# Optimization experiments

Measured on AMD Instinct MI355X. Metric: run time of the kernel, lower is better.

The kernel has to match this reference:

```python
import jax, jax.numpy as jnp
import numpy as np
import math

E = 256          # embed_dims
H = 8            # num_heads
ITER = 2         # iterative steps
PC_RANGE = (-140.8, -40.0, -3.0, 140.8, 40.0, 1.0)


def sine_embed(pos, num_feats):
    # pos: (..., 3) in (0,1); returns (..., 3*num_feats), per-coord interleaved sin/cos
    scale = 2.0 * math.pi
    i = jnp.arange(num_feats, dtype=jnp.float32)
    dim_t = 10000.0 ** (2.0 * jnp.floor(i / 2.0) / num_feats)
    p = pos[..., None] * scale / dim_t                      # (..., 3, F)
    emb = jnp.stack([jnp.sin(p[..., 0::2]), jnp.cos(p[..., 1::2])], axis=-1)
    emb = emb.reshape(p.shape[:-1] + (num_feats,))          # (..., 3, F)
    return emb.reshape(pos.shape[:-1] + (3 * num_feats,))


def mha(q, k, v, Wi, bi, Wo, bo, n_heads):
    # torch nn.MultiheadAttention math, seq-first layout: q (L,N,C), k/v (M,N,C)
    L, N, C = q.shape
    D = C // n_heads
    qp = (q @ Wi[:C].T + bi[:C]).reshape(L, N, n_heads, D)
    kp = (k @ Wi[C:2 * C].T + bi[C:2 * C]).reshape(k.shape[0], N, n_heads, D)
    vp = (v @ Wi[2 * C:].T + bi[2 * C:]).reshape(v.shape[0], N, n_heads, D)
    scores = jnp.einsum('lnhd,mnhd->nhlm', qp, kp) / math.sqrt(D)
    attn = jax.nn.softmax(scores, axis=-1)
    o = jnp.einsum('nhlm,mnhd->lnhd', attn, vp).reshape(L, N, C)
    return o @ Wo.T + bo


def setup_inputs() -> dict:
    key = jax.random.key(0)
    ks = jax.random.split(key, 12)
    Q, TOT, B, LMAX = 2048, 40, 8, 5
    s = 0.02
    return {
        'x': jax.random.normal(ks[0], (Q, TOT, E), jnp.float32),
        'reference_points': jax.random.uniform(ks[1], (TOT, Q, 3), jnp.float32),
        'pairwise_t_matrix': jax.random.normal(ks[2], (B, LMAX, LMAX, 4, 4), jnp.float32),
        'record_len': np.full((B,), 5, dtype=np.int64),
        'in_proj_w': jax.random.normal(ks[3], (3 * E, E), jnp.float32) * s,
        'in_proj_b': jnp.zeros((3 * E,), jnp.float32),
        'out_w': jax.random.normal(ks[4], (E, E), jnp.float32) * s,
        'out_b': jnp.zeros((E,), jnp.float32),
        'bev_w1': jax.random.normal(ks[5], (E, 3 * E), jnp.float32) * s,
        'bev_b1': jnp.zeros((E,), jnp.float32),
        'bev_w2': jax.random.normal(ks[6], (E, E), jnp.float32) * s,
        'bev_b2': jnp.zeros((E,), jnp.float32),
    }


def reference(x, reference_points, pairwise_t_matrix, in_proj_w, in_proj_b,
              out_w, out_b, bev_w1, bev_b1, bev_w2, bev_b2, record_len):
    rl = np.asarray(record_len)
    offsets = np.concatenate([[0], np.cumsum(rl)]).astype(int)
    lo = jnp.asarray(PC_RANGE[:3], jnp.float32)
    hi = jnp.asarray(PC_RANGE[3:], jnp.float32)

    x_cav = jnp.transpose(x, (1, 0, 2))                    # (total_cav, Q, C)
    ref = reference_points * (hi - lo) + lo                # un-normalize to pc_range

    outs = []
    for b in range(len(rl)):
        s, e = offsets[b], offsets[b + 1]
        n = e - s
        b_x = x_cav[s:e]                                   # (n, Q, C)
        if n == 1:
            outs.append(b_x)
            continue
        b_ref = ref[s:e]                                   # (n, Q, 3)
        t_ego = pairwise_t_matrix[b, :n, 0]                # (n, 4, 4) transform-to-ego
        homo = jnp.concatenate([b_ref, jnp.ones(b_ref.shape[:-1] + (1,), b_ref.dtype)], axis=-1)
        trans = jax.nn.sigmoid(jnp.einsum('nij,nqj->nqi', t_ego, homo)[..., :3])
        pe = sine_embed(trans, E)                          # (n, Q, 3E)
        bev = jax.nn.relu(pe @ bev_w1.T + bev_b1) @ bev_w2.T + bev_b2  # (n, Q, C)

        ego = b_x[0:1]
        neigh = b_x[1:]                                    # (n-1, Q, C)
        kk = neigh + bev[1:]
        for _ in range(ITER):
            q = jnp.broadcast_to(ego, neigh.shape)
            o = q + mha(q, kk, neigh, in_proj_w, in_proj_b, out_w, out_b, H)
            ego = jnp.sum(o, axis=0, keepdims=True)
        outs.append(jnp.concatenate([ego, neigh], axis=0))

    out = jnp.concatenate(outs, axis=0)                    # (total_cav, Q, C)
    return jnp.transpose(out, (1, 0, 2))                   # (Q, total_cav, C)
```

## Files before the change

kernel.cpp:

```cpp
#include <hip/hip_runtime.h>
#include <cstdint>
#include <cstddef>

typedef __bf16 bf16;
typedef __attribute__((ext_vector_type(8))) __bf16 bf16x8;
typedef __attribute__((ext_vector_type(4))) float f32x4;
typedef __attribute__((ext_vector_type(4))) unsigned int u32x4;

#define QN 2048

#if __has_builtin(__builtin_amdgcn_sinf)
#define SIN_REV(x) __builtin_amdgcn_sinf(x)
#define COS_REV(x) __builtin_amdgcn_cosf(x)
#else
#define SIN_REV(x) __sinf((x) * 6.283185307179586f)
#define COS_REV(x) __cosf((x) * 6.283185307179586f)
#endif

__device__ __forceinline__ float sigmoidf_(float v) { return 1.0f / (1.0f + __expf(-v)); }

__device__ __forceinline__ bf16x8 cvt8(const float* p) {
  const f32x4* p4 = (const f32x4*)p;
  f32x4 lo = p4[0], hi = p4[1];
  bf16x8 r;
#pragma unroll
  for (int j = 0; j < 4; ++j) { r[j] = (bf16)lo[j]; r[j + 4] = (bf16)hi[j]; }
  return r;
}

__device__ __forceinline__ void load_lds16(const bf16* g, bf16* l) {
  __builtin_amdgcn_global_load_lds(
      (const __attribute__((address_space(1))) void*)g,
      (__attribute__((address_space(3))) void*)l, 16, 0, 0);
}

__global__ __launch_bounds__(256) void setup_ker(
    const float* __restrict__ ipw, const float* __restrict__ ow,
    const float* __restrict__ w1, bf16* __restrict__ wb,
    const float* __restrict__ ipb, const float* __restrict__ w2f,
    const float* __restrict__ b2f, bf16* __restrict__ Wc,
    float* __restrict__ bkf) {
  __shared__ float row[256];
  __shared__ float red[256];
  if (blockIdx.x < 224) {
    int e = (blockIdx.x * 256 + threadIdx.x) * 8;
    const float* src; int off;
    if (e < 196608)      { src = ipw; off = e; }
    else if (e < 262144) { src = ow;  off = e - 196608; }
    else                 { src = w1;  off = e - 262144; }
    *(bf16x8*)(wb + e) = cvt8(src + off);
    return;
  }
  const int j = blockIdx.x - 224, l = threadIdx.x;
  row[l] = ipw[65536 + j * 256 + l];
  __syncthreads();
  float acc = 0.f;
#pragma unroll 4
  for (int m = 0; m < 256; ++m) acc += row[m] * w2f[m * 256 + l];
  Wc[(size_t)j * 512 + l] = (bf16)acc;
  Wc[(size_t)j * 512 + 256 + l] = (bf16)row[l];
  red[l] = row[l] * b2f[l];
  __syncthreads();
  for (int s = 128; s > 0; s >>= 1) {
    if (l < s) red[l] += red[l + s];
    __syncthreads();
  }
  if (l == 0) bkf[j] = ipb[256 + j] + red[0];
}

__global__ __launch_bounds__(256) void mega_ker(
    const bf16* __restrict__ w1b, const float* __restrict__ b1,
    const bf16* __restrict__ Wc, const float* __restrict__ bkf,
    const bf16* __restrict__ wv, const float* __restrict__ bv,
    const float* __restrict__ x, const float* __restrict__ rp,
    const float* __restrict__ pm, bf16* __restrict__ kp,
    bf16* __restrict__ vp, float* __restrict__ out) {
  __shared__ bf16 As[64][40];
  __shared__ bf16 Bs[256][32];
  __shared__ bf16 hT[64][256];

  const int tid = threadIdx.x;
  const int wave = tid >> 6, lane = tid & 63;
  const int m16 = lane & 15, quad = lane >> 4;
  const int sRow = tid >> 2, sq = tid & 3;

  if (blockIdx.x >= 2048) {
    for (int i = (blockIdx.x - 2048) * 256 + tid; i < 5242880; i += 524288) {
      int t = (i >> 6) % 40;
      if ((t % 5) != 0) ((u32x4*)out)[i] = ((const u32x4*)x)[i];
    }
    return;
  }

  const bool isPE = blockIdx.x < 1024;
  const int rowBase = (isPE ? blockIdx.x : blockIdx.x - 1024) << 6;
  const int rgA = rowBase + sRow;
  const int b = rgA >> 13, j = (rgA >> 11) & 3, q = rgA & 2047;
  const float* afp = x + (((size_t)q * 40 + b * 5 + 1 + j) << 8);

  f32x4 acc[4][4] = {};

  if (isPE) {
    const int t = b * 5 + 1 + j;
    const float* rpp = rp + ((size_t)t * QN + q) * 3;
    float r0 = rpp[0] * 281.6f - 140.8f;
    float r1 = rpp[1] * 80.0f - 40.0f;
    float r2 = rpp[2] * 4.0f - 3.0f;
    const float* T = pm + (size_t)t * 80;
    const float tr0 = sigmoidf_(T[0] * r0 + T[1] * r1 + T[2] * r2 + T[3]);
    const float tr1 = sigmoidf_(T[4] * r0 + T[5] * r1 + T[6] * r2 + T[7]);
    const float tr2 = sigmoidf_(T[8] * r0 + T[9] * r1 + T[10] * r2 + T[11]);

    const bf16* ws1 = w1b + (size_t)((wave << 6) + (lane >> 2)) * 768 + ((lane & 3) << 3);
    for (int k0 = 0; k0 < 768; k0 += 32) {
#pragma unroll
      for (int i = 0; i < 4; ++i)
        load_lds16(ws1 + (size_t)(i << 4) * 768 + k0, &Bs[(wave << 6) + (i << 4)][0]);
      bf16x8 a0;
      {
        int c = k0 >> 8;
        float tc = (c == 0) ? tr0 : (c == 1 ? tr1 : tr2);
        int ti0 = ((k0 & 255) + (sq << 3)) >> 1;
        float freq = exp2f((float)ti0 * -0.10381025296522975f);
#pragma unroll
        for (int p = 0; p < 4; ++p) {
          float ang = tc * freq;
          a0[2 * p]     = (bf16)SIN_REV(ang);
          a0[2 * p + 1] = (bf16)COS_REV(ang);
          freq *= 0.93057204092467f;
        }
      }
      *(bf16x8*)(&As[sRow][sq << 3]) = a0;
      __syncthreads();
      bf16x8 afr[4], bfr[4];
#pragma unroll
      for (int mt = 0; mt < 4; ++mt)
        afr[mt] = *(const bf16x8*)(&As[(mt << 4) + m16][quad << 3]);
#pragma unroll
      for (int nt = 0; nt < 4; ++nt)
        bfr[nt] = *(const bf16x8*)(&Bs[(wave << 6) + (nt << 4) + m16][quad << 3]);
#pragma unroll
      for (int mt = 0; mt < 4; ++mt)
#pragma unroll
        for (int nt = 0; nt < 4; ++nt)
          acc[mt][nt] = __builtin_amdgcn_mfma_f32_16x16x32_bf16(
              afr[mt], bfr[nt], acc[mt][nt], 0, 0, 0);
      __syncthreads();
    }
#pragma unroll
    for (int mt = 0; mt < 4; ++mt)
#pragma unroll
      for (int nt = 0; nt < 4; ++nt) {
        const int col = (wave << 6) + (nt << 4) + m16;
        const float bvv = b1[col];
#pragma unroll
        for (int rg = 0; rg < 4; ++rg) {
          const int row = (mt << 4) + (quad << 2) + rg;
          hT[row][((((col >> 3) ^ (row & 7)) << 3) + (col & 7))] =
              (bf16)fmaxf(acc[mt][nt][rg] + bvv, 0.0f);
        }
      }
    __syncthreads();

#pragma unroll
    for (int mt = 0; mt < 4; ++mt)
#pragma unroll
      for (int nt = 0; nt < 4; ++nt) {
        f32x4 z = {0.f, 0.f, 0.f, 0.f};
        acc[mt][nt] = z;
      }
    const bf16* ws2 = Wc + (size_t)((wave << 6) + (lane >> 2)) * 512 + ((lane & 3) << 3);
    for (int k0 = 0; k0 < 512; k0 += 32) {
#pragma unroll
      for (int i = 0; i < 4; ++i)
        load_lds16(ws2 + (size_t)(i << 4) * 512 + k0, &Bs[(wave << 6) + (i << 4)][0]);
      if (k0 >= 256) {
        bf16x8 a0 = cvt8(afp + (k0 - 256) + (sq << 3));
        *(bf16x8*)(&As[sRow][sq << 3]) = a0;
      }
      __syncthreads();
      bf16x8 afr[4], bfr[4];
      if (k0 < 256) {
#pragma unroll
        for (int mt = 0; mt < 4; ++mt) {
          const int row = (mt << 4) + m16;
          afr[mt] = *(const bf16x8*)(
              &hT[row][((((k0 >> 3) + quad) ^ (row & 7)) << 3)]);
        }
      } else {
#pragma unroll
        for (int mt = 0; mt < 4; ++mt)
          afr[mt] = *(const bf16x8*)(&As[(mt << 4) + m16][quad << 3]);
      }
#pragma unroll
      for (int nt = 0; nt < 4; ++nt)
        bfr[nt] = *(const bf16x8*)(&Bs[(wave << 6) + (nt << 4) + m16][quad << 3]);
#pragma unroll
      for (int mt = 0; mt < 4; ++mt)
#pragma unroll
        for (int nt = 0; nt < 4; ++nt)
          acc[mt][nt] = __builtin_amdgcn_mfma_f32_16x16x32_bf16(
              afr[mt], bfr[nt], acc[mt][nt], 0, 0, 0);
      __syncthreads();
    }
#pragma unroll
    for (int mt = 0; mt < 4; ++mt)
#pragma unroll
      for (int nt = 0; nt < 4; ++nt) {
        const int col = (wave << 6) + (nt << 4) + m16;
        const float bvv = bkf[col];
#pragma unroll
        for (int rg = 0; rg < 4; ++rg) {
          const int r = rowBase + (mt << 4) + (quad << 2) + rg;
          kp[(size_t)r * 256 + col] = (bf16)(acc[mt][nt][rg] + bvv);
        }
      }
    return;
  }

  const bf16* wsV = wv + (size_t)((wave << 6) + (lane >> 2)) * 256 + ((lane & 3) << 3);
  for (int k0 = 0; k0 < 256; k0 += 32) {
#pragma unroll
    for (int i = 0; i < 4; ++i)
      load_lds16(wsV + (size_t)(i << 4) * 256 + k0, &Bs[(wave << 6) + (i << 4)][0]);
    bf16x8 a0 = cvt8(afp + k0 + (sq << 3));
    *(bf16x8*)(&As[sRow][sq << 3]) = a0;
    __syncthreads();
    bf16x8 afr[4], bfr[4];
#pragma unroll
    for (int mt = 0; mt < 4; ++mt)
      afr[mt] = *(const bf16x8*)(&As[(mt << 4) + m16][quad << 3]);
#pragma unroll
    for (int nt = 0; nt < 4; ++nt)
      bfr[nt] = *(const bf16x8*)(&Bs[(wave << 6) + (nt << 4) + m16][quad << 3]);
#pragma unroll
    for (int mt = 0; mt < 4; ++mt)
#pragma unroll
      for (int nt = 0; nt < 4; ++nt)
        acc[mt][nt] = __builtin_amdgcn_mfma_f32_16x16x32_bf16(
            afr[mt], bfr[nt], acc[mt][nt], 0, 0, 0);
    __syncthreads();
  }
#pragma unroll
  for (int mt = 0; mt < 4; ++mt)
#pragma unroll
    for (int nt = 0; nt < 4; ++nt) {
      const int col = (wave << 6) + (nt << 4) + m16;
      const float bvv = bv[col];
#pragma unroll
      for (int rg = 0; rg < 4; ++rg) {
        const int r = rowBase + (mt << 4) + (quad << 2) + rg;
        vp[(size_t)r * 256 + col] = (bf16)(acc[mt][nt][rg] + bvv);
      }
    }
}

__device__ __forceinline__ void proj32db(const bf16 (*AP)[256],
                                         bf16 (*BsP)[256][32],
                                         const bf16* __restrict__ WB,
                                         f32x4 (*acc)[4], int wave, int lane) {
  const int m16 = lane & 15, quad = lane >> 4;
#define PSTAGE(P_, K_)                                                        \
  { _Pragma("unroll") for (int i_ = 0; i_ < 4; ++i_) {                        \
      const bf16* src_ = WB +                                                 \
          (size_t)((wave << 6) + (i_ << 4) + (lane >> 2)) * 256 + (K_) +      \
          ((lane & 3) << 3);                                                  \
      load_lds16(src_, &BsP[P_][(wave << 6) + (i_ << 4)][0]); } }
  PSTAGE(0, 0);
#pragma unroll
  for (int t = 0; t < 8; ++t) {
    const int p = t & 1;
    if (t < 7) {
      PSTAGE(p ^ 1, (t + 1) << 5);
      asm volatile("s_waitcnt vmcnt(4)" ::: "memory");
    } else {
      asm volatile("s_waitcnt vmcnt(0)" ::: "memory");
    }
    __builtin_amdgcn_sched_barrier(0);
    const int k0 = t << 5;
    bf16x8 afr[2], bfr[4];
#pragma unroll
    for (int mt = 0; mt < 2; ++mt) {
      const int r = (mt << 4) + m16;
      afr[mt] = *(const bf16x8*)(&AP[r][(((k0 >> 3) + quad) ^ (r & 7)) << 3]);
    }
#pragma unroll
    for (int nt = 0; nt < 4; ++nt)
      bfr[nt] = *(const bf16x8*)(&BsP[p][(wave << 6) + (nt << 4) + m16][quad << 3]);
#pragma unroll
    for (int mt = 0; mt < 2; ++mt)
#pragma unroll
      for (int nt = 0; nt < 4; ++nt)
        acc[mt][nt] = __builtin_amdgcn_mfma_f32_16x16x32_bf16(
            afr[mt], bfr[nt], acc[mt][nt], 0, 0, 0);
  }
#undef PSTAGE
}

__device__ __forceinline__ void attn_phase(bf16 (*P)[256],
                                           const bf16* __restrict__ kp,
                                           const bf16* __restrict__ vp,
                                           int rowBase, int tid) {
  const int r = tid >> 3, h = tid & 7;
  const int re = rowBase + r, b = re >> 11, q = re & 2047;
  float qv[32];
#pragma unroll
  for (int i = 0; i < 4; ++i) {
    bf16x8 t = *(const bf16x8*)(&P[r][((((h << 2) + i)) ^ (r & 7)) << 3]);
#pragma unroll
    for (int j = 0; j < 8; ++j) qv[i * 8 + j] = (float)t[j];
  }
  const size_t base = ((size_t)(b * 4) * QN + q) * 256 + h * 32;
  float s[4];
#pragma unroll
  for (int m = 0; m < 4; ++m) {
    const bf16x8* kv = (const bf16x8*)(kp + base + (size_t)m * (QN * 256));
    float a = 0.f;
#pragma unroll
    for (int i = 0; i < 4; ++i) {
      bf16x8 t = kv[i];
#pragma unroll
      for (int j = 0; j < 8; ++j) a += qv[i * 8 + j] * (float)t[j];
    }
    s[m] = a * 0.17677669529663687f;
  }
  float mx = fmaxf(fmaxf(s[0], s[1]), fmaxf(s[2], s[3]));
  float e0 = __expf(s[0] - mx), e1 = __expf(s[1] - mx);
  float e2 = __expf(s[2] - mx), e3 = __expf(s[3] - mx);
  float inv = 1.0f / (e0 + e1 + e2 + e3);
  float w[4] = {e0 * inv, e1 * inv, e2 * inv, e3 * inv};
  float ov[32] = {};
#pragma unroll
  for (int m = 0; m < 4; ++m) {
    const bf16x8* vv = (const bf16x8*)(vp + base + (size_t)m * (QN * 256));
#pragma unroll
    for (int i = 0; i < 4; ++i) {
      bf16x8 t = vv[i];
#pragma unroll
      for (int j = 0; j < 8; ++j) ov[i * 8 + j] += w[m] * (float)t[j];
    }
  }
#pragma unroll
  for (int i = 0; i < 4; ++i) {
    bf16x8 t;
#pragma unroll
    for (int j = 0; j < 8; ++j) t[j] = (bf16)ov[i * 8 + j];
    *(bf16x8*)(&P[r][((((h << 2) + i)) ^ (r & 7)) << 3]) = t;
  }
}

__global__ __launch_bounds__(256, 2) void iter_ker(
    const bf16* __restrict__ kp, const bf16* __restrict__ vp,
    const bf16* __restrict__ wq, const bf16* __restrict__ owb,
    const float* __restrict__ qb, const float* __restrict__ ob,
    const float* __restrict__ x, float* __restrict__ out) {
  __shared__ bf16 P1[32][256];
  __shared__ bf16 P2[32][256];
  __shared__ bf16 Bs[2][256][32];

  const int tid = threadIdx.x;
  const int rowBase = blockIdx.x << 5;
  const int wave = tid >> 6, lane = tid & 63;
  const int m16 = lane & 15, quad = lane >> 4;

  {
    const int r = tid >> 3, e = tid & 7;
    const int re = rowBase + r, b = re >> 11, q = re & 2047;
    const float* src = x + (((size_t)q * 40 + b * 5) << 8) + (e << 5);
#pragma unroll
    for (int s = 0; s < 4; ++s) {
      bf16x8 v = cvt8(src + s * 8);
      *(bf16x8*)(&P1[r][((((e << 2) + s)) ^ (r & 7)) << 3]) = v;
    }
  }
  __syncthreads();

  float e1r[2][4][4];
  f32x4 acc[2][4];

#define ZACC                                                                  \
  { _Pragma("unroll") for (int mt = 0; mt < 2; ++mt)                          \
    _Pragma("unroll") for (int nt = 0; nt < 4; ++nt) {                        \
      f32x4 z = {0.f, 0.f, 0.f, 0.f}; acc[mt][nt] = z; } }

#define QEPI                                                                  \
  { _Pragma("unroll") for (int mt = 0; mt < 2; ++mt)                          \
    _Pragma("unroll") for (int nt = 0; nt < 4; ++nt) {                        \
      const int col = (wave << 6) + (nt << 4) + m16;                          \
      const float bv = qb[col];                                               \
      _Pragma("unroll") for (int rg = 0; rg < 4; ++rg) {                      \
        const int row = (mt << 4) + (quad << 2) + rg;                         \
        P2[row][(((col >> 3) ^ (row & 7)) << 3) + (col & 7)] =                \
            (bf16)(acc[mt][nt][rg] + bv);                                     \
      } } }

  ZACC;
  proj32db(P1, Bs, wq, acc, wave, lane);
  QEPI;
  __syncthreads();
  attn_phase(P2, kp, vp, rowBase, tid);
  __syncthreads();
  ZACC;
  proj32db(P2, Bs, owb, acc, wave, lane);
#pragma unroll
  for (int mt = 0; mt < 2; ++mt)
#pragma unroll
    for (int nt = 0; nt < 4; ++nt) {
      const int col = (wave << 6) + (nt << 4) + m16;
      const float bv = ob[col];
#pragma unroll
      for (int rg = 0; rg < 4; ++rg) {
        const int row = (mt << 4) + (quad << 2) + rg;
        const int re = rowBase + row, b = re >> 11, q = re & 2047;
        float xe = x[(((size_t)q * 40 + b * 5) << 8) + col];
        float e1 = 4.0f * (xe + acc[mt][nt][rg] + bv);
        e1r[mt][nt][rg] = e1;
        P1[row][(((col >> 3) ^ (row & 7)) << 3) + (col & 7)] = (bf16)e1;
      }
    }
  __syncthreads();

  ZACC;
  proj32db(P1, Bs, wq, acc, wave, lane);
  QEPI;
  __syncthreads();
  attn_phase(P2, kp, vp, rowBase, tid);
  __syncthreads();
  ZACC;
  proj32db(P2, Bs, owb, acc, wave, lane);
#pragma unroll
  for (int mt = 0; mt < 2; ++mt)
#pragma unroll
    for (int nt = 0; nt < 4; ++nt) {
      const int col = (wave << 6) + (nt << 4) + m16;
      const float bv = ob[col];
#pragma unroll
      for (int rg = 0; rg < 4; ++rg) {
        const int row = (mt << 4) + (quad << 2) + rg;
        const int re = rowBase + row, b = re >> 11, q = re & 2047;
        out[(((size_t)q * 40 + b * 5) << 8) + col] =
            4.0f * (e1r[mt][nt][rg] + acc[mt][nt][rg] + bv);
      }
    }
#undef ZACC
#undef QEPI
}

extern "C" void kernel_launch(void* const* d_in, const int* in_sizes, int n_in,
                              void* d_out, int out_size, void* d_ws, size_t ws_size,
                              hipStream_t stream) {
  (void)n_in; (void)out_size; (void)ws_size;
  const float* x   = (const float*)d_in[0];
  const float* rp  = (const float*)d_in[1];
  const float* pm  = (const float*)d_in[2];
  const int wbase = (in_sizes[3] == 8) ? 4 : 3;
  const float* ipw = (const float*)d_in[wbase + 0];
  const float* ipb = (const float*)d_in[wbase + 1];
  const float* ow  = (const float*)d_in[wbase + 2];
  const float* obv = (const float*)d_in[wbase + 3];
  const float* w1  = (const float*)d_in[wbase + 4];
  const float* b1  = (const float*)d_in[wbase + 5];
  const float* w2  = (const float*)d_in[wbase + 6];
  const float* b2  = (const float*)d_in[wbase + 7];
  float* out = (float*)d_out;
  char* ws = (char*)d_ws;

  bf16* kp   = (bf16*)(ws + 33554432);
  bf16* vp   = (bf16*)(ws + 67108864);
  bf16* wb   = (bf16*)(ws + 100663296);
  bf16* Wc   = (bf16*)(ws + 101711872);
  float* bkf = (float*)(ws + 101974016);
  const bf16* wq  = wb;
  const bf16* wv  = wb + 131072;
  const bf16* owb = wb + 196608;
  const bf16* w1b = wb + 262144;

  setup_ker<<<480, 256, 0, stream>>>(ipw, ow, w1, wb, ipb, w2, b2, Wc, bkf);
  mega_ker<<<4096, 256, 0, stream>>>(w1b, b1, Wc, bkf, wv, ipb + 512,
                                     x, rp, pm, kp, vp, out);
  iter_ker<<<512, 256, 0, stream>>>(kp, vp, wq, owb, ipb, obv, x, out);
}
```

Measured before the change: 341.0 us.

## Double-buffer weight tiles and compute sine features in registers to drop barriers

The PE GEMM phases now double-buffer the per-wave B tiles in shared memory and prefetch the next k-slice while computing the current one. Because each wave reads only the B rows it loaded itself, the block barriers are replaced by vmcnt waits. The sine/cosine positional features are computed straight into MFMA A-fragments per lane rather than staged through shared memory. This removes per-iteration __syncthreads and the LDS round trip, at the cost of redundant transcendental work per lane (4 rows each), extra LDS for the second buffer, and reliance on hand-written waitcnt ordering.

```diff
diff --git a/kernel.cpp b/kernel.cpp
--- a/kernel.cpp
+++ b/kernel.cpp
@@ -76,7 +76,7 @@
     const float* __restrict__ pm, bf16* __restrict__ kp,
     bf16* __restrict__ vp, float* __restrict__ out) {
   __shared__ bf16 As[64][40];
-  __shared__ bf16 Bs[256][32];
+  __shared__ bf16 BsD[2][256][32];
   __shared__ bf16 hT[64][256];
 
   const int tid = threadIdx.x;
@@ -94,59 +94,70 @@
 
   const bool isPE = blockIdx.x < 1024;
   const int rowBase = (isPE ? blockIdx.x : blockIdx.x - 1024) << 6;
-  const int rgA = rowBase + sRow;
-  const int b = rgA >> 13, j = (rgA >> 11) & 3, q = rgA & 2047;
-  const float* afp = x + (((size_t)q * 40 + b * 5 + 1 + j) << 8);
 
   f32x4 acc[4][4] = {};
 
   if (isPE) {
-    const int t = b * 5 + 1 + j;
-    const float* rpp = rp + ((size_t)t * QN + q) * 3;
-    float r0 = rpp[0] * 281.6f - 140.8f;
-    float r1 = rpp[1] * 80.0f - 40.0f;
-    float r2 = rpp[2] * 4.0f - 3.0f;
-    const float* T = pm + (size_t)t * 80;
-    const float tr0 = sigmoidf_(T[0] * r0 + T[1] * r1 + T[2] * r2 + T[3]);
-    const float tr1 = sigmoidf_(T[4] * r0 + T[5] * r1 + T[6] * r2 + T[7]);
-    const float tr2 = sigmoidf_(T[8] * r0 + T[9] * r1 + T[10] * r2 + T[11]);
+    float trL[3][4];
+#pragma unroll
+    for (int mt = 0; mt < 4; ++mt) {
+      const int rr = rowBase + (mt << 4) + m16;
+      const int bb = rr >> 13, jj = (rr >> 11) & 3, qq = rr & 2047;
+      const int tt = bb * 5 + 1 + jj;
+      const float* rpp = rp + ((size_t)tt * QN + qq) * 3;
+      float r0 = rpp[0] * 281.6f - 140.8f;
+      float r1 = rpp[1] * 80.0f - 40.0f;
+      float r2 = rpp[2] * 4.0f - 3.0f;
+      const float* T = pm + (size_t)tt * 80;
+      trL[0][mt] = sigmoidf_(T[0] * r0 + T[1] * r1 + T[2] * r2 + T[3]);
+      trL[1][mt] = sigmoidf_(T[4] * r0 + T[5] * r1 + T[6] * r2 + T[7]);
+      trL[2][mt] = sigmoidf_(T[8] * r0 + T[9] * r1 + T[10] * r2 + T[11]);
+    }
 
     const bf16* ws1 = w1b + (size_t)((wave << 6) + (lane >> 2)) * 768 + ((lane & 3) << 3);
-    for (int k0 = 0; k0 < 768; k0 += 32) {
-#pragma unroll
-      for (int i = 0; i < 4; ++i)
-        load_lds16(ws1 + (size_t)(i << 4) * 768 + k0, &Bs[(wave << 6) + (i << 4)][0]);
-      bf16x8 a0;
-      {
-        int c = k0 >> 8;
-        float tc = (c == 0) ? tr0 : (c == 1 ? tr1 : tr2);
-        int ti0 = ((k0 & 255) + (sq << 3)) >> 1;
-        float freq = exp2f((float)ti0 * -0.10381025296522975f);
-#pragma unroll
-        for (int p = 0; p < 4; ++p) {
+#define STG1(P_, K_)                                                          \
+    { _Pragma("unroll") for (int i_ = 0; i_ < 4; ++i_)                        \
+        load_lds16(ws1 + (size_t)(i_ << 4) * 768 + (K_),                      \
+                   &BsD[P_][(wave << 6) + (i_ << 4)][0]); }
+    STG1(0, 0);
+#pragma unroll
+    for (int t = 0; t < 24; ++t) {
+      const int p = t & 1;
+      if (t < 23) {
+        STG1(p ^ 1, (t + 1) << 5);
+        asm volatile("s_waitcnt vmcnt(4)" ::: "memory");
+      } else {
+        asm volatile("s_waitcnt vmcnt(0)" ::: "memory");
+      }
+      __builtin_amdgcn_sched_barrier(0);
+      const int k0 = t << 5;
+      const int c = k0 >> 8;
+      bf16x8 afr[4], bfr[4];
+#pragma unroll
+      for (int mt = 0; mt < 4; ++mt) {
+        const float tc = trL[c][mt];
+        float freq = exp2f((float)((((k0 & 255)) + (quad << 3)) >> 1) *
+                           -0.10381025296522975f);
+#pragma unroll
+        for (int pp = 0; pp < 4; ++pp) {
           float ang = tc * freq;
-          a0[2 * p]     = (bf16)SIN_REV(ang);
-          a0[2 * p + 1] = (bf16)COS_REV(ang);
+          afr[mt][2 * pp]     = (bf16)SIN_REV(ang);
+          afr[mt][2 * pp + 1] = (bf16)COS_REV(ang);
           freq *= 0.93057204092467f;
         }
       }
-      *(bf16x8*)(&As[sRow][sq << 3]) = a0;
-      __syncthreads();
-      bf16x8 afr[4], bfr[4];
-#pragma unroll
-      for (int mt = 0; mt < 4; ++mt)
-        afr[mt] = *(const bf16x8*)(&As[(mt << 4) + m16][quad << 3]);
 #pragma unroll
       for (int nt = 0; nt < 4; ++nt)
-        bfr[nt] = *(const bf16x8*)(&Bs[(wave << 6) + (nt << 4) + m16][quad << 3]);
+        bfr[nt] = *(const bf16x8*)(&BsD[p][(wave << 6) + (nt << 4) + m16][quad << 3]);
 #pragma unroll
       for (int mt = 0; mt < 4; ++mt)
 #pragma unroll
         for (int nt = 0; nt < 4; ++nt)
           acc[mt][nt] = __builtin_amdgcn_mfma_f32_16x16x32_bf16(
               afr[mt], bfr[nt], acc[mt][nt], 0, 0, 0);
-      __syncthreads();
-    }
+    }
+#undef STG1
+
 #pragma unroll
     for (int mt = 0; mt < 4; ++mt)
 #pragma unroll
@@ -170,38 +181,68 @@
         acc[mt][nt] = z;
       }
     const bf16* ws2 = Wc + (size_t)((wave << 6) + (lane >> 2)) * 512 + ((lane & 3) << 3);
-    for (int k0 = 0; k0 < 512; k0 += 32) {
-#pragma unroll
-      for (int i = 0; i < 4; ++i)
-        load_lds16(ws2 + (size_t)(i << 4) * 512 + k0, &Bs[(wave << 6) + (i << 4)][0]);
-      if (k0 >= 256) {
-        bf16x8 a0 = cvt8(afp + (k0 - 256) + (sq << 3));
-        *(bf16x8*)(&As[sRow][sq << 3]) = a0;
-      }
-      __syncthreads();
+#define STG2(P_, K_)                                                          \
+    { _Pragma("unroll") for (int i_ = 0; i_ < 4; ++i_)                        \
+        load_lds16(ws2 + (size_t)(i_ << 4) * 512 + (K_),                      \
+                   &BsD[P_][(wave << 6) + (i_ << 4)][0]); }
+    STG2(0, 0);
+#pragma unroll
+    for (int t = 0; t < 8; ++t) {
+      const int p = t & 1;
+      if (t < 7) {
+        STG2(p ^ 1, (t + 1) << 5);
+        asm volatile("s_waitcnt vmcnt(4)" ::: "memory");
+      } else {
+        asm volatile("s_waitcnt vmcnt(0)" ::: "memory");
+      }
+      __builtin_amdgcn_sched_barrier(0);
+      const int k0 = t << 5;
       bf16x8 afr[4], bfr[4];
-      if (k0 < 256) {
-#pragma unroll
-        for (int mt = 0; mt < 4; ++mt) {
-          const int row = (mt << 4) + m16;
-          afr[mt] = *(const bf16x8*)(
-              &hT[row][((((k0 >> 3) + quad) ^ (row & 7)) << 3)]);
-        }
-      } else {
-#pragma unroll
-        for (int mt = 0; mt < 4; ++mt)
-          afr[mt] = *(const bf16x8*)(&As[(mt << 4) + m16][quad << 3]);
+#pragma unroll
+      for (int mt = 0; mt < 4; ++mt) {
+        const int row = (mt << 4) + m16;
+        afr[mt] = *(const bf16x8*)(
+            &hT[row][((((k0 >> 3) + quad) ^ (row & 7)) << 3)]);
       }
 #pragma unroll
       for (int nt = 0; nt < 4; ++nt)
-        bfr[nt] = *(const bf16x8*)(&Bs[(wave << 6) + (nt << 4) + m16][quad << 3]);
+        bfr[nt] = *(const bf16x8*)(&BsD[p][(wave << 6) + (nt << 4) + m16][quad << 3]);
 #pragma unroll
       for (int mt = 0; mt < 4; ++mt)
 #pragma unroll
         for (int nt = 0; nt < 4; ++nt)
           acc[mt][nt] = __builtin_amdgcn_mfma_f32_16x16x32_bf16(
               afr[mt], bfr[nt], acc[mt][nt], 0, 0, 0);
-      __syncthreads();
+    }
+#undef STG2
+
+    {
+      const int rgA = rowBase + sRow;
+      const int b = rgA >> 13, j = (rgA >> 11) & 3, q = rgA & 2047;
+      const float* afp = x + (((size_t)q * 40 + b * 5 + 1 + j) << 8);
+      for (int k0 = 256; k0 < 512; k0 += 32) {
+#pragma unroll
+        for (int i = 0; i < 4; ++i)
+          load_lds16(ws2 + (size_t)(i << 4) * 512 + k0,
+                     &BsD[0][(wave << 6) + (i << 4)][0]);
+        bf16x8 a0 = cvt8(afp + (k0 - 256) + (sq << 3));
+        *(bf16x8*)(&As[sRow][sq << 3]) = a0;
+        __syncthreads();
+        bf16x8 afr[4], bfr[4];
+#pragma unroll
+        for (int mt = 0; mt < 4; ++mt)
+          afr[mt] = *(const bf16x8*)(&As[(mt << 4) + m16][quad << 3]);
+#pragma unroll
+        for (int nt = 0; nt < 4; ++nt)
+          bfr[nt] = *(const bf16x8*)(&BsD[0][(wave << 6) + (nt << 4) + m16][quad << 3]);
+#pragma unroll
+        for (int mt = 0; mt < 4; ++mt)
+#pragma unroll
+          for (int nt = 0; nt < 4; ++nt)
+            acc[mt][nt] = __builtin_amdgcn_mfma_f32_16x16x32_bf16(
+                afr[mt], bfr[nt], acc[mt][nt], 0, 0, 0);
+        __syncthreads();
+      }
     }
 #pragma unroll
     for (int mt = 0; mt < 4; ++mt)
@@ -218,11 +259,15 @@
     return;
   }
 
+  const int rgA = rowBase + sRow;
+  const int b = rgA >> 13, j = (rgA >> 11) & 3, q = rgA & 2047;
+  const float* afp = x + (((size_t)q * 40 + b * 5 + 1 + j) << 8);
   const bf16* wsV = wv + (size_t)((wave << 6) + (lane >> 2)) * 256 + ((lane & 3) << 3);
   for (int k0 = 0; k0 < 256; k0 += 32) {
 #pragma unroll
     for (int i = 0; i < 4; ++i)
-      load_lds16(wsV + (size_t)(i << 4) * 256 + k0, &Bs[(wave << 6) + (i << 4)][0]);
+      load_lds16(wsV + (size_t)(i << 4) * 256 + k0,
+                 &BsD[0][(wave << 6) + (i << 4)][0]);
     bf16x8 a0 = cvt8(afp + k0 + (sq << 3));
     *(bf16x8*)(&As[sRow][sq << 3]) = a0;
     __syncthreads();
@@ -232,7 +277,7 @@
       afr[mt] = *(const bf16x8*)(&As[(mt << 4) + m16][quad << 3]);
 #pragma unroll
     for (int nt = 0; nt < 4; ++nt)
-      bfr[nt] = *(const bf16x8*)(&Bs[(wave << 6) + (nt << 4) + m16][quad << 3]);
+      bfr[nt] = *(const bf16x8*)(&BsD[0][(wave << 6) + (nt << 4) + m16][quad << 3]);
 #pragma unroll
     for (int mt = 0; mt < 4; ++mt)
 #pragma unroll
```

New measurement: 332.6 us (median of 2 runs). -2.5%, faster.
